# Kernel tuning notes

Measured on AMD Instinct MI355X. Metric: run time of the kernel, lower is better.

The kernel has to match this reference:

```python
import jax, jax.numpy as jnp
import numpy as np

B, S, D, H = 2, 2048, 1024, 16
DK = D // H
ROPE_BASE = 10000.0


def setup_inputs() -> dict:
    key = jax.random.key(0)
    ks = jax.random.split(key, 6)
    x = jax.random.normal(ks[0], (B, S, D), dtype=jnp.float32)
    # causal mask, broadcastable to [B,H,S,S]; masked_fill where mask==0
    mask = jnp.tril(jnp.ones((S, S), dtype=bool))[None, None]
    position_ids = jnp.tile(jnp.arange(S, dtype=jnp.int32)[None, :], (B, 1))
    sc = 1.0 / np.sqrt(D)
    Wq = jax.random.normal(ks[1], (D, D), dtype=jnp.float32) * sc
    Wk = jax.random.normal(ks[2], (D, D), dtype=jnp.float32) * sc
    Wv = jax.random.normal(ks[3], (D, D), dtype=jnp.float32) * sc
    Wo = jax.random.normal(ks[4], (D, D), dtype=jnp.float32) * sc
    bo = jnp.zeros((D,), dtype=jnp.float32)
    return {"x": x, "mask": mask, "position_ids": position_ids,
            "Wq": Wq, "Wk": Wk, "Wv": Wv, "Wo": Wo, "bo": bo}


def _rotate_half(t):
    t1, t2 = t[..., : t.shape[-1] // 2], t[..., t.shape[-1] // 2:]
    return jnp.concatenate((-t2, t1), axis=-1)


def reference(x, mask, position_ids, Wq, Wk, Wv, Wo, bo):
    b, s, d = x.shape
    h, dk = H, DK
    scale = 1.0 / np.sqrt(dk)

    def proj(W):  # torch Linear: x @ W.T -> [b,h,s,dk]
        return (x @ W.T).reshape(b, s, h, dk).transpose(0, 2, 1, 3)

    Q, K, V = proj(Wq), proj(Wk), proj(Wv)

    # rotary tables (computed in fp32, matching RotaryEmbedding)
    inv_freq = 1.0 / (ROPE_BASE ** (jnp.arange(0, dk, 2, dtype=jnp.float32) / dk))
    t = jnp.arange(s, dtype=jnp.float32)
    freqs = jnp.outer(t, inv_freq)            # [s, dk/2]
    emb = jnp.concatenate((freqs, freqs), -1) # [s, dk]
    cos = jnp.cos(emb)[position_ids][:, None]  # [b,1,s,dk]
    sin = jnp.sin(emb)[position_ids][:, None]
    Q = Q * cos + _rotate_half(Q) * sin
    K = K * cos + _rotate_half(K) * sin

    scores = jnp.einsum('bhqd,bhkd->bhqk', Q, K) * scale
    scores = jnp.where(mask, scores, jnp.float32(-1e9))
    attn = jax.nn.softmax(scores, axis=-1)  # dropout is identity in eval
    out = jnp.einsum('bhqk,bhkd->bhqd', attn, V)
    out = out.transpose(0, 2, 1, 3).reshape(b, s, d)
    return out @ Wo.T + bo
```

## Files before the change

### kernel.cpp

```cpp
#include <hip/hip_runtime.h>
#include <hip/hip_bf16.h>
#include <cstdint>

#define BB 2
#define SS 2048
#define DD 1024
#define HH 16
#define DK 64
#define MROWS (BB*SS)
#define NQKV  (3*DD)

typedef __bf16 bf16x8 __attribute__((ext_vector_type(8)));
typedef float  f32x4  __attribute__((ext_vector_type(4)));
typedef float  f32x16 __attribute__((ext_vector_type(16)));
typedef unsigned u32x2 __attribute__((ext_vector_type(2)));

static __device__ __forceinline__ unsigned short f2bf(float f) {
    __bf16 h = (__bf16)f;
    return __builtin_bit_cast(unsigned short, h);
}
static __device__ __forceinline__ float bf2f(unsigned short u) {
    return (float)__builtin_bit_cast(__bf16, u);
}

#define GLOAD16(gsrc, ldst) \
    __builtin_amdgcn_global_load_lds((const __attribute__((address_space(1))) void*)(gsrc), \
                                     (__attribute__((address_space(3))) void*)(ldst), 16, 0, 0)

static __device__ __forceinline__ void pl32_swap(unsigned &x, unsigned &y) {
#if __has_builtin(__builtin_amdgcn_permlane32_swap)
    u32x2 r = __builtin_amdgcn_permlane32_swap(x, y, false, false);
    x = r[0]; y = r[1];
#else
    asm volatile("v_permlane32_swap_b32 %0, %1" : "+v"(x), "+v"(y));
#endif
}
static __device__ __forceinline__ float swap_half(float v, bool hi) {
    unsigned x = __builtin_bit_cast(unsigned, v), y = x;
    pl32_swap(x, y);
    return __builtin_bit_cast(float, hi ? x : y);
}
template<int BASE> static __device__ __forceinline__ bf16x8 cvt_chunk(const f32x16 &p) {
    unsigned x0, y0, x1, y1;
    asm("v_cvt_pk_bf16_f32 %0, %1, %2" : "=v"(x0) : "v"(p[BASE+0]), "v"(p[BASE+1]));
    asm("v_cvt_pk_bf16_f32 %0, %1, %2" : "=v"(y0) : "v"(p[BASE+4]), "v"(p[BASE+5]));
    asm("v_cvt_pk_bf16_f32 %0, %1, %2" : "=v"(x1) : "v"(p[BASE+2]), "v"(p[BASE+3]));
    asm("v_cvt_pk_bf16_f32 %0, %1, %2" : "=v"(y1) : "v"(p[BASE+6]), "v"(p[BASE+7]));
    pl32_swap(x0, y0);
    pl32_swap(x1, y1);
    union { unsigned u[4]; bf16x8 v; } r;
    r.u[0] = x0; r.u[1] = x1; r.u[2] = y0; r.u[3] = y1;
    return r.v;
}

__global__ void cast_all(const float* __restrict__ x,  const float* __restrict__ wq,
                         const float* __restrict__ wk, const float* __restrict__ wv,
                         const float* __restrict__ wo,
                         unsigned short* __restrict__ xb, unsigned short* __restrict__ wqkv,
                         unsigned short* __restrict__ wob)
{
    const int NX = MROWS * DD;
    const int NW = DD * DD;
    const int total = (NX + 4 * NW) / 8;
    for (int i = blockIdx.x * blockDim.x + threadIdx.x; i < total; i += gridDim.x * blockDim.x) {
        int base = i * 8;
        const float* src; unsigned short* dst; int off;
        if      (base < NX)          { src = x;  dst = xb;          off = base; }
        else if (base < NX + NW)     { src = wq; dst = wqkv;        off = base - NX; }
        else if (base < NX + 2*NW)   { src = wk; dst = wqkv + NW;   off = base - NX - NW; }
        else if (base < NX + 3*NW)   { src = wv; dst = wqkv + 2*NW; off = base - NX - 2*NW; }
        else                         { src = wo; dst = wob;         off = base - NX - 3*NW; }
        float4 a = *(const float4*)(src + off);
        float4 b = *(const float4*)(src + off + 4);
        union { unsigned short s[8]; uint4 v; } u;
        u.s[0] = f2bf(a.x); u.s[1] = f2bf(a.y); u.s[2] = f2bf(a.z); u.s[3] = f2bf(a.w);
        u.s[4] = f2bf(b.x); u.s[5] = f2bf(b.y); u.s[6] = f2bf(b.z); u.s[7] = f2bf(b.w);
        *(uint4*)(dst + off) = u.v;
    }
}

__global__ void rope_table(float* __restrict__ tabc, float* __restrict__ tabs)
{
    int i = blockIdx.x * blockDim.x + threadIdx.x;
    int s = i >> 5, d = i & 31;
    float inv = exp2f(-(float)d * (13.287712379549449f / 32.f));
    float ang = (float)s * inv;
    tabc[i] = cosf(ang);
    tabs[i] = sinf(ang);
}

__global__ __launch_bounds__(512) void gemm_qkv(
    const unsigned short* __restrict__ A, const unsigned short* __restrict__ Bm,
    const int* __restrict__ pids,
    const float* __restrict__ tabc, const float* __restrict__ tabs,
    unsigned short* __restrict__ Qb, unsigned short* __restrict__ Kb,
    unsigned short* __restrict__ Vr)
{
    __shared__ __align__(16) unsigned short sA[2][16384];
    __shared__ __align__(16) unsigned short sB[2][16384];
    const int tid = threadIdx.x;
    const int w = tid >> 6, l = tid & 63;
    const int wm = w >> 2, wn = w & 3;
    const int lr = l & 15, lg = l >> 4;
    const int swz = (blockIdx.x & 7) * 24 + (blockIdx.x >> 3);
    const int bx = swz % 12, by = swz / 12;
    const int mBase = by * 256;
    const int sr  = tid >> 3;
    const int scb = (tid & 7) * 8;
    const int sksw = scb ^ ((sr & 7) * 8);
    const int rdsw = (lr & 7) * 8;

    f32x4 acc[8][4] = {};

    auto stage = [&](int kt, int bb) {
        #pragma unroll
        for (int r = 0; r < 4; ++r) {
            GLOAD16(A  + (size_t)(mBase + r*64 + sr) * DD + kt + sksw,
                    &sA[bb][r*4096 + sr*64 + scb]);
            GLOAD16(Bm + (size_t)(bx*256 + r*64 + sr) * DD + kt + sksw,
                    &sB[bb][r*4096 + sr*64 + scb]);
        }
    };

    stage(0, 0);
    __syncthreads();

    for (int t = 0; t < 16; ++t) {
        const int cur = t & 1;
        #pragma unroll
        for (int p = 0; p < 4; ++p) {
            const int rh = p & 1, ks = p >> 1;
            bf16x8 af[4], bfv[4];
            #pragma unroll
            for (int rf = 0; rf < 4; ++rf) {
                int ra = wm*128 + rh*64 + rf*16 + lr;
                af[rf] = *(const bf16x8*)&sA[cur][ra*64 + ((ks*32 + lg*8) ^ rdsw)];
            }
            #pragma unroll
            for (int cf = 0; cf < 4; ++cf) {
                int rb = wn*64 + cf*16 + lr;
                bfv[cf] = *(const bf16x8*)&sB[cur][rb*64 + ((ks*32 + lg*8) ^ rdsw)];
            }
            if (p == 0 && t < 15) stage((t+1)*64, cur ^ 1);
            __builtin_amdgcn_s_barrier();
            __builtin_amdgcn_s_setprio(1);
            #pragma unroll
            for (int rf = 0; rf < 4; ++rf)
                #pragma unroll
                for (int cf = 0; cf < 4; ++cf)
                    acc[rh*4+rf][cf] = __builtin_amdgcn_mfma_f32_16x16x32_bf16(
                        af[rf], bfv[cf], acc[rh*4+rf][cf], 0, 0, 0);
            __builtin_amdgcn_s_setprio(0);
            if (p < 3) __builtin_amdgcn_s_barrier();
        }
        __syncthreads();
    }

    if (bx < 8) {
        const bool isQ = bx < 4;
        unsigned short* dst = isQ ? Qb : Kb;
        const float qsc = isQ ? 0.1803368801111244f : 1.0f;
        const int colbase = (bx & 3)*256 + wn*64;
        #pragma unroll
        for (int rr = 0; rr < 8; ++rr) {
            #pragma unroll
            for (int j = 0; j < 4; ++j) {
                int row = mBase + wm*128 + rr*16 + lg*4 + j;
                int pos = pids[row];
                #pragma unroll
                for (int cf = 0; cf < 2; ++cf) {
                    int d = cf*16 + lr;
                    float cc = tabc[pos*32 + d];
                    float sn = tabs[pos*32 + d];
                    float a  = acc[rr][cf][j];
                    float bb2 = acc[rr][cf+2][j];
                    dst[(size_t)row * DD + colbase + d]      = f2bf((a*cc - bb2*sn) * qsc);
                    dst[(size_t)row * DD + colbase + d + 32] = f2bf((bb2*cc + a*sn) * qsc);
                }
            }
        }
    } else {
        const int colbase = (bx - 8)*256 + wn*64;
        #pragma unroll
        for (int rr = 0; rr < 8; ++rr) {
            #pragma unroll
            for (int j = 0; j < 4; ++j) {
                int row = mBase + wm*128 + rr*16 + lg*4 + j;
                #pragma unroll
                for (int cf = 0; cf < 4; ++cf)
                    Vr[(size_t)row * DD + colbase + cf*16 + lr] = f2bf(acc[rr][cf][j]);
            }
        }
    }
}

__global__ __launch_bounds__(256) void gemm_bt(
    const unsigned short* __restrict__ A, const unsigned short* __restrict__ Bm,
    float* __restrict__ Cout, const float* __restrict__ bias,
    int M, int N, int K)
{
    __shared__ __align__(16) unsigned short sA[2][128 * 64];
    __shared__ __align__(16) unsigned short sB[2][128 * 64];
    const int tid = threadIdx.x;
    const int w = tid >> 6, l = tid & 63;
    const int wm = w >> 1, wn = w & 1;
    const int lr = l & 15, lg = l >> 4;
    const int nwg = gridDim.x;
    const int cpx = nwg >> 3;
    const int swz = (blockIdx.x & 7) * cpx + (blockIdx.x >> 3);
    const int nbx = N >> 7;
    const int bx = swz % nbx, by = swz / nbx;
    const int mBase = by * 128, nBase = bx * 128;
    const int srow = tid >> 3;
    const int skof = (tid & 7) * 8;

    f32x4 acc[4][4] = {};

    #pragma unroll
    for (int i = 0; i < 4; ++i) {
        GLOAD16(A  + (size_t)(mBase + i*32 + srow) * K + skof, &sA[0][i*2048 + w*512]);
        GLOAD16(Bm + (size_t)(nBase + i*32 + srow) * K + skof, &sB[0][i*2048 + w*512]);
    }
    int cur = 0;

    for (int kt = 0; kt < K; kt += 64) {
        __syncthreads();
        if (kt + 64 < K) {
            #pragma unroll
            for (int i = 0; i < 4; ++i) {
                GLOAD16(A  + (size_t)(mBase + i*32 + srow) * K + kt + 64 + skof, &sA[cur^1][i*2048 + w*512]);
                GLOAD16(Bm + (size_t)(nBase + i*32 + srow) * K + kt + 64 + skof, &sB[cur^1][i*2048 + w*512]);
            }
        }
        #pragma unroll
        for (int kk = 0; kk < 2; ++kk) {
            bf16x8 af[4], bfv[4];
            #pragma unroll
            for (int mi = 0; mi < 4; ++mi)
                af[mi] = *(const bf16x8*)&sA[cur][(wm*64 + mi*16 + lr)*64 + kk*32 + lg*8];
            #pragma unroll
            for (int ni = 0; ni < 4; ++ni)
                bfv[ni] = *(const bf16x8*)&sB[cur][(wn*64 + ni*16 + lr)*64 + kk*32 + lg*8];
            #pragma unroll
            for (int mi = 0; mi < 4; ++mi)
                #pragma unroll
                for (int ni = 0; ni < 4; ++ni)
                    acc[mi][ni] = __builtin_amdgcn_mfma_f32_16x16x32_bf16(af[mi], bfv[ni], acc[mi][ni], 0, 0, 0);
        }
        cur ^= 1;
    }
    #pragma unroll
    for (int mi = 0; mi < 4; ++mi) {
        #pragma unroll
        for (int j = 0; j < 4; ++j) {
            int row = mBase + wm*64 + mi*16 + lg*4 + j;
            #pragma unroll
            for (int ni = 0; ni < 4; ++ni) {
                int col = nBase + wn*64 + ni*16 + lr;
                Cout[(size_t)row * N + col] = acc[mi][ni][j] + bias[col];
            }
        }
    }
}

__global__ __launch_bounds__(256) void v_transpose(
    const unsigned short* __restrict__ Vr, unsigned short* __restrict__ Vt)
{
    __shared__ __align__(16) unsigned short sT[64 * 64];
    const int bh = blockIdx.y;
    const int st = blockIdx.x;
    const int b = bh >> 4, h = bh & 15;
    const int tid = threadIdx.x;
    #pragma unroll
    for (int i = 0; i < 2; ++i) {
        int c = tid + i*256;
        int s = c >> 3, cb = c & 7;
        const unsigned short* src = Vr + (size_t)(b*SS + st*64 + s) * DD + h*64 + cb*8;
        uint4 v = *(const uint4*)src;
        *(uint4*)&sT[s*64 + ((cb ^ (s >> 3)) * 8)] = v;
    }
    __syncthreads();
    #pragma unroll
    for (int i = 0; i < 2; ++i) {
        int c = tid + i*256;
        int d = c >> 3, sb = c & 7;
        union { unsigned short u[8]; uint4 v; } o;
        #pragma unroll
        for (int e = 0; e < 8; ++e) {
            int s = sb*8 + e;
            o.u[e] = sT[s*64 + (((d >> 3) ^ (s >> 3)) * 8) + (d & 7)];
        }
        *(uint4*)(Vt + (size_t)(bh*64 + d) * SS + st*64 + sb*8) = o.v;
    }
}

__global__ __launch_bounds__(256, 2) void attn_fwd(
    const unsigned short* __restrict__ Qb,
    const unsigned short* __restrict__ Kb,
    const unsigned short* __restrict__ Vt,
    unsigned short* __restrict__ Ob)
{
    __shared__ __align__(16) unsigned short sK[2][8192];
    __shared__ __align__(16) unsigned short sV[2][8192];
    const int tid = threadIdx.x;
    const int w = tid >> 6, l = tid & 63;
    const int lq = l & 31;
    const int hi5 = l >> 5;
    const bool hb = hi5 != 0;

    const int xcd  = blockIdx.x & 7;
    const int c    = blockIdx.x >> 3;
    const int gsel = c & 3;
    const int t    = c >> 2;
    const int qt   = (t < 8) ? t : 23 - t;
    const int bh   = xcd * 4 + gsel;
    const int b = bh >> 4, h = bh & 15;

    const int srow = tid >> 3;
    const int skof = (tid & 7) * 8;
    const int sksw = skof ^ ((srow & 7) * 8);
    const int sw   = (lq & 7) * 8;
    const float THR = 12.0f;

    bf16x8 qf[4];
    {
        const unsigned short* qp = Qb + (size_t)(b*SS + qt*128 + w*32 + lq) * DD + h*64 + hi5*8;
        #pragma unroll
        for (int dkc = 0; dkc < 4; ++dkc)
            qf[dkc] = *(const bf16x8*)(qp + dkc*16);
    }
    const int q_lane = qt*128 + w*32 + lq;
    const int wbase  = qt*128 + w*32;

    f32x16 o0 = {}, o1 = {};
    float mrow = -3.0e38f, lsum = 0.f;
    int cur = 0;

    auto stage = [&](int ktt, int bb) {
        #pragma unroll
        for (int r = 0; r < 4; ++r)
            GLOAD16(Kb + (size_t)(b*SS + ktt*128 + r*32 + srow) * DD + h*64 + sksw,
                    &sK[bb][r*2048 + w*512]);
        #pragma unroll
        for (int s = 0; s < 2; ++s)
            #pragma unroll
            for (int r = 0; r < 2; ++r)
                GLOAD16(Vt + (size_t)(bh*64 + r*32 + srow) * SS + ktt*128 + s*64 + sksw,
                        &sV[bb][s*4096 + r*2048 + w*512]);
    };

    stage(0, 0);

    for (int ktt = 0; ktt <= qt; ++ktt) {
        __syncthreads();
        if (ktt < qt) stage(ktt + 1, cur ^ 1);

        f32x16 pa0 = {}, pa1 = {};
        f32x16 pb0 = {}, pb1 = {};
        __builtin_amdgcn_s_setprio(1);
        #pragma unroll
        for (int dkc = 0; dkc < 4; ++dkc) {
            bf16x8 k0 = *(const bf16x8*)&sK[cur][lq*64 + ((dkc*16 + hi5*8) ^ sw)];
            pa0 = __builtin_amdgcn_mfma_f32_32x32x16_bf16(k0, qf[dkc], pa0, 0, 0, 0);
        }
        #pragma unroll
        for (int dkc = 0; dkc < 4; ++dkc) {
            bf16x8 k1 = *(const bf16x8*)&sK[cur][2048 + lq*64 + ((dkc*16 + hi5*8) ^ sw)];
            pa1 = __builtin_amdgcn_mfma_f32_32x32x16_bf16(k1, qf[dkc], pa1, 0, 0, 0);
        }
        #pragma unroll
        for (int dkc = 0; dkc < 4; ++dkc) {
            bf16x8 k2 = *(const bf16x8*)&sK[cur][4096 + lq*64 + ((dkc*16 + hi5*8) ^ sw)];
            pb0 = __builtin_amdgcn_mfma_f32_32x32x16_bf16(k2, qf[dkc], pb0, 0, 0, 0);
        }
        #pragma unroll
        for (int dkc = 0; dkc < 4; ++dkc) {
            bf16x8 k3 = *(const bf16x8*)&sK[cur][4096 + 2048 + lq*64 + ((dkc*16 + hi5*8) ^ sw)];
            pb1 = __builtin_amdgcn_mfma_f32_32x32x16_bf16(k3, qf[dkc], pb1, 0, 0, 0);
        }
        __builtin_amdgcn_s_setprio(0);

        {
            const int kt = 2*ktt;
            if (kt*64 + 63 > wbase) {
                const int kb0 = kt*64 + 4*hi5;
                #pragma unroll
                for (int r = 0; r < 16; ++r) {
                    const int cr = (r & 3) + 8*(r >> 2);
                    if (kb0 + cr > q_lane)      pa0[r] = -1e30f;
                    if (kb0 + 32 + cr > q_lane) pa1[r] = -1e30f;
                }
            }
            float tt[16];
            #pragma unroll
            for (int r = 0; r < 16; ++r) tt[r] = fmaxf(pa0[r], pa1[r]);
            #pragma unroll
            for (int s2 = 8; s2 >= 1; s2 >>= 1)
                #pragma unroll
                for (int r = 0; r < 8; ++r)
                    if (r < s2) tt[r] = fmaxf(tt[r], tt[r + s2]);
            float tmx = fmaxf(tt[0], swap_half(tt[0], hb));
            float growth = tmx - mrow;
            if (!__all(growth <= THR)) {
                float mnew = fmaxf(mrow, tmx);
                float alpha = exp2f(mrow - mnew);
                lsum *= alpha;
                mrow = mnew;
                #pragma unroll
                for (int r = 0; r < 16; ++r) { o0[r] *= alpha; o1[r] *= alpha; }
            }
            #pragma unroll
            for (int r = 0; r < 16; ++r) {
                pa0[r] = exp2f(pa0[r] - mrow);
                pa1[r] = exp2f(pa1[r] - mrow);
            }
            float st[16];
            #pragma unroll
            for (int r = 0; r < 16; ++r) st[r] = pa0[r] + pa1[r];
            #pragma unroll
            for (int s2 = 8; s2 >= 1; s2 >>= 1)
                #pragma unroll
                for (int r = 0; r < 8; ++r)
                    if (r < s2) st[r] += st[r + s2];
            lsum += st[0];
        }

        __builtin_amdgcn_s_setprio(1);
        {
            bf16x8 pv, vf;
            pv = cvt_chunk<0>(pa0);
            vf = *(const bf16x8*)&sV[cur][lq*64 + ((0*16 + hi5*8) ^ sw)];
            o0 = __builtin_amdgcn_mfma_f32_32x32x16_bf16(vf, pv, o0, 0, 0, 0);
            vf = *(const bf16x8*)&sV[cur][2048 + lq*64 + ((0*16 + hi5*8) ^ sw)];
            o1 = __builtin_amdgcn_mfma_f32_32x32x16_bf16(vf, pv, o1, 0, 0, 0);
            pv = cvt_chunk<8>(pa0);
            vf = *(const bf16x8*)&sV[cur][lq*64 + ((1*16 + hi5*8) ^ sw)];
            o0 = __builtin_amdgcn_mfma_f32_32x32x16_bf16(vf, pv, o0, 0, 0, 0);
            vf = *(const bf16x8*)&sV[cur][2048 + lq*64 + ((1*16 + hi5*8) ^ sw)];
            o1 = __builtin_amdgcn_mfma_f32_32x32x16_bf16(vf, pv, o1, 0, 0, 0);
            pv = cvt_chunk<0>(pa1);
            vf = *(const bf16x8*)&sV[cur][lq*64 + ((2*16 + hi5*8) ^ sw)];
            o0 = __builtin_amdgcn_mfma_f32_32x32x16_bf16(vf, pv, o0, 0, 0, 0);
            vf = *(const bf16x8*)&sV[cur][2048 + lq*64 + ((2*16 + hi5*8) ^ sw)];
            o1 = __builtin_amdgcn_mfma_f32_32x32x16_bf16(vf, pv, o1, 0, 0, 0);
            pv = cvt_chunk<8>(pa1);
            vf = *(const bf16x8*)&sV[cur][lq*64 + ((3*16 + hi5*8) ^ sw)];
            o0 = __builtin_amdgcn_mfma_f32_32x32x16_bf16(vf, pv, o0, 0, 0, 0);
            vf = *(const bf16x8*)&sV[cur][2048 + lq*64 + ((3*16 + hi5*8) ^ sw)];
            o1 = __builtin_amdgcn_mfma_f32_32x32x16_bf16(vf, pv, o1, 0, 0, 0);
        }
        __builtin_amdgcn_s_setprio(0);

        {
            const int kt = 2*ktt + 1;
            if (kt*64 + 63 > wbase) {
                const int kb0 = kt*64 + 4*hi5;
                #pragma unroll
                for (int r = 0; r < 16; ++r) {
                    const int cr = (r & 3) + 8*(r >> 2);
                    if (kb0 + cr > q_lane)      pb0[r] = -1e30f;
                    if (kb0 + 32 + cr > q_lane) pb1[r] = -1e30f;
                }
            }
            float tt[16];
            #pragma unroll
            for (int r = 0; r < 16; ++r) tt[r] = fmaxf(pb0[r], pb1[r]);
            #pragma unroll
            for (int s2 = 8; s2 >= 1; s2 >>= 1)
                #pragma unroll
                for (int r = 0; r < 8; ++r)
                    if (r < s2) tt[r] = fmaxf(tt[r], tt[r + s2]);
            float tmx = fmaxf(tt[0], swap_half(tt[0], hb));
            float growth = tmx - mrow;
            if (!__all(growth <= THR)) {
                float mnew = fmaxf(mrow, tmx);
                float alpha = exp2f(mrow - mnew);
                lsum *= alpha;
                mrow = mnew;
                #pragma unroll
                for (int r = 0; r < 16; ++r) { o0[r] *= alpha; o1[r] *= alpha; }
            }
            #pragma unroll
            for (int r = 0; r < 16; ++r) {
                pb0[r] = exp2f(pb0[r] - mrow);
                pb1[r] = exp2f(pb1[r] - mrow);
            }
            float st[16];
            #pragma unroll
            for (int r = 0; r < 16; ++r) st[r] = pb0[r] + pb1[r];
            #pragma unroll
            for (int s2 = 8; s2 >= 1; s2 >>= 1)
                #pragma unroll
                for (int r = 0; r < 8; ++r)
                    if (r < s2) st[r] += st[r + s2];
            lsum += st[0];
        }

        __builtin_amdgcn_s_setprio(1);
        {
            bf16x8 pv, vf;
            pv = cvt_chunk<0>(pb0);
            vf = *(const bf16x8*)&sV[cur][4096 + lq*64 + ((0*16 + hi5*8) ^ sw)];
            o0 = __builtin_amdgcn_mfma_f32_32x32x16_bf16(vf, pv, o0, 0, 0, 0);
            vf = *(const bf16x8*)&sV[cur][4096 + 2048 + lq*64 + ((0*16 + hi5*8) ^ sw)];
            o1 = __builtin_amdgcn_mfma_f32_32x32x16_bf16(vf, pv, o1, 0, 0, 0);
            pv = cvt_chunk<8>(pb0);
            vf = *(const bf16x8*)&sV[cur][4096 + lq*64 + ((1*16 + hi5*8) ^ sw)];
            o0 = __builtin_amdgcn_mfma_f32_32x32x16_bf16(vf, pv, o0, 0, 0, 0);
            vf = *(const bf16x8*)&sV[cur][4096 + 2048 + lq*64 + ((1*16 + hi5*8) ^ sw)];
            o1 = __builtin_amdgcn_mfma_f32_32x32x16_bf16(vf, pv, o1, 0, 0, 0);
            pv = cvt_chunk<0>(pb1);
            vf = *(const bf16x8*)&sV[cur][4096 + lq*64 + ((2*16 + hi5*8) ^ sw)];
            o0 = __builtin_amdgcn_mfma_f32_32x32x16_bf16(vf, pv, o0, 0, 0, 0);
            vf = *(const bf16x8*)&sV[cur][4096 + 2048 + lq*64 + ((2*16 + hi5*8) ^ sw)];
            o1 = __builtin_amdgcn_mfma_f32_32x32x16_bf16(vf, pv, o1, 0, 0, 0);
            pv = cvt_chunk<8>(pb1);
            vf = *(const bf16x8*)&sV[cur][4096 + lq*64 + ((3*16 + hi5*8) ^ sw)];
            o0 = __builtin_amdgcn_mfma_f32_32x32x16_bf16(vf, pv, o0, 0, 0, 0);
            vf = *(const bf16x8*)&sV[cur][4096 + 2048 + lq*64 + ((3*16 + hi5*8) ^ sw)];
            o1 = __builtin_amdgcn_mfma_f32_32x32x16_bf16(vf, pv, o1, 0, 0, 0);
        }
        __builtin_amdgcn_s_setprio(0);
        cur ^= 1;
    }

    __syncthreads();
    float ls = lsum + swap_half(lsum, hb);
    float inv = 1.f / ls;
    unsigned short* sOw = &sK[0][0] + w * 2048;

    #pragma unroll
    for (int g2 = 0; g2 < 4; ++g2) {
        unsigned ua, ub; uint2 t2;
        float v0 = o0[g2*4+0]*inv, v1 = o0[g2*4+1]*inv, v2 = o0[g2*4+2]*inv, v3 = o0[g2*4+3]*inv;
        asm("v_cvt_pk_bf16_f32 %0, %1, %2" : "=v"(ua) : "v"(v0), "v"(v1));
        asm("v_cvt_pk_bf16_f32 %0, %1, %2" : "=v"(ub) : "v"(v2), "v"(v3));
        t2.x = ua; t2.y = ub;
        *(uint2*)&sOw[lq*64 + g2*8 + hi5*4] = t2;
        float w0 = o1[g2*4+0]*inv, w1 = o1[g2*4+1]*inv, w2 = o1[g2*4+2]*inv, w3 = o1[g2*4+3]*inv;
        asm("v_cvt_pk_bf16_f32 %0, %1, %2" : "=v"(ua) : "v"(w0), "v"(w1));
        asm("v_cvt_pk_bf16_f32 %0, %1, %2" : "=v"(ub) : "v"(w2), "v"(w3));
        t2.x = ua; t2.y = ub;
        *(uint2*)&sOw[lq*64 + 32 + g2*8 + hi5*4] = t2;
    }
    asm volatile("s_waitcnt lgkmcnt(0)" ::: "memory");
    __builtin_amdgcn_sched_barrier(0);

    const int row = l >> 1, cb2 = (l & 1) * 32;
    const unsigned short* sOr = sOw + row*64 + cb2;
    unsigned short* gp = Ob + (size_t)(b*SS + qt*128 + w*32 + row) * DD + h*64 + cb2;
    #pragma unroll
    for (int c2 = 0; c2 < 4; ++c2)
        *(uint4*)(gp + c2*8) = *(const uint4*)(sOr + c2*8);
}

extern "C" void kernel_launch(void* const* d_in, const int* in_sizes, int n_in,
                              void* d_out, int out_size, void* d_ws, size_t ws_size,
                              hipStream_t stream)
{
    const float* x  = (const float*)d_in[0];
    const int* pids = (const int*)d_in[2];
    const float* wq = (const float*)d_in[3];
    const float* wk = (const float*)d_in[4];
    const float* wv = (const float*)d_in[5];
    const float* wo = (const float*)d_in[6];
    const float* bo = (const float*)d_in[7];
    float* out = (float*)d_out;

    char* ws = (char*)d_ws;
    unsigned short* xb   = (unsigned short*)(ws);
    unsigned short* wqkv = (unsigned short*)(ws + (size_t)( 8u<<20));
    unsigned short* wob  = (unsigned short*)(ws + (size_t)(14u<<20));
    unsigned short* Vr   = (unsigned short*)(ws + (size_t)(16u<<20));
    unsigned short* Qb   = (unsigned short*)(ws + (size_t)(40u<<20));
    unsigned short* Kb   = (unsigned short*)(ws + (size_t)(48u<<20));
    unsigned short* Vt   = (unsigned short*)(ws + (size_t)(56u<<20));
    float* tabc          = (float*)(ws + (size_t)(64u<<20));
    float* tabs          = (float*)(ws + (size_t)(64u<<20) + (256u<<10));
    unsigned short* Ob   = xb;

    cast_all<<<dim3(4096), dim3(256), 0, stream>>>(x, wq, wk, wv, wo, xb, wqkv, wob);
    rope_table<<<dim3(256), dim3(256), 0, stream>>>(tabc, tabs);
    gemm_qkv<<<dim3(192), dim3(512), 0, stream>>>(
        xb, wqkv, pids, tabc, tabs, Qb, Kb, Vr);
    v_transpose<<<dim3(32, 32), dim3(256), 0, stream>>>(Vr, Vt);
    attn_fwd<<<dim3(512), dim3(256), 0, stream>>>(Qb, Kb, Vt, Ob);
    gemm_bt<<<dim3(256), dim3(256), 0, stream>>>(
        Ob, wob, out, bo, MROWS, DD, DD);
}
```

Baseline: 133.9 us.

## Deepen QKV GEMM pipeline to four-slot K=32 ring with vmcnt waits

Replaces the double-buffered K=64 staging in the QKV projection GEMM with a four-slot ring of K=32 tiles, keeping three loads in flight. It uses s_waitcnt vmcnt counting and one barrier per step instead of full __syncthreads, and changes the LDS swizzle to fit 32-wide rows. The aim is to hide global-load latency better and cut synchronisation overhead. In exchange there are twice as many iterations, and the code relies on the vmcnt count matching the number of outstanding loads.

```diff
diff --git a/kernel.cpp b/kernel.cpp
--- a/kernel.cpp
+++ b/kernel.cpp
@@ -96,8 +96,8 @@
     unsigned short* __restrict__ Qb, unsigned short* __restrict__ Kb,
     unsigned short* __restrict__ Vr)
 {
-    __shared__ __align__(16) unsigned short sA[2][16384];
-    __shared__ __align__(16) unsigned short sB[2][16384];
+    __shared__ __align__(16) unsigned short sA[4][8192];
+    __shared__ __align__(16) unsigned short sB[4][8192];
     const int tid = threadIdx.x;
     const int w = tid >> 6, l = tid & 63;
     const int wm = w >> 2, wn = w & 3;
@@ -105,55 +105,51 @@
     const int swz = (blockIdx.x & 7) * 24 + (blockIdx.x >> 3);
     const int bx = swz % 12, by = swz / 12;
     const int mBase = by * 256;
-    const int sr  = tid >> 3;
-    const int scb = (tid & 7) * 8;
-    const int sksw = scb ^ ((sr & 7) * 8);
-    const int rdsw = (lr & 7) * 8;
+    const int nBase = bx * 256;
+    const int srow = tid >> 2;
+    const int schw = tid & 3;
 
     f32x4 acc[8][4] = {};
 
-    auto stage = [&](int kt, int bb) {
-        #pragma unroll
-        for (int r = 0; r < 4; ++r) {
-            GLOAD16(A  + (size_t)(mBase + r*64 + sr) * DD + kt + sksw,
-                    &sA[bb][r*4096 + sr*64 + scb]);
-            GLOAD16(Bm + (size_t)(bx*256 + r*64 + sr) * DD + kt + sksw,
-                    &sB[bb][r*4096 + sr*64 + scb]);
+    auto stage = [&](int kh) {
+        const int slot = kh & 3;
+        const int kbase = kh * 32;
+        #pragma unroll
+        for (int r = 0; r < 2; ++r) {
+            int row = r * 128 + srow;
+            int scol = kbase + ((schw ^ ((row >> 1) & 3)) * 8);
+            GLOAD16(A  + (size_t)(mBase + row) * DD + scol, &sA[slot][r*4096 + tid*8]);
+            GLOAD16(Bm + (size_t)(nBase + row) * DD + scol, &sB[slot][r*4096 + tid*8]);
         }
     };
 
-    stage(0, 0);
-    __syncthreads();
-
-    for (int t = 0; t < 16; ++t) {
-        const int cur = t & 1;
-        #pragma unroll
-        for (int p = 0; p < 4; ++p) {
-            const int rh = p & 1, ks = p >> 1;
-            bf16x8 af[4], bfv[4];
-            #pragma unroll
-            for (int rf = 0; rf < 4; ++rf) {
-                int ra = wm*128 + rh*64 + rf*16 + lr;
-                af[rf] = *(const bf16x8*)&sA[cur][ra*64 + ((ks*32 + lg*8) ^ rdsw)];
-            }
-            #pragma unroll
-            for (int cf = 0; cf < 4; ++cf) {
-                int rb = wn*64 + cf*16 + lr;
-                bfv[cf] = *(const bf16x8*)&sB[cur][rb*64 + ((ks*32 + lg*8) ^ rdsw)];
-            }
-            if (p == 0 && t < 15) stage((t+1)*64, cur ^ 1);
-            __builtin_amdgcn_s_barrier();
-            __builtin_amdgcn_s_setprio(1);
-            #pragma unroll
-            for (int rf = 0; rf < 4; ++rf)
-                #pragma unroll
-                for (int cf = 0; cf < 4; ++cf)
-                    acc[rh*4+rf][cf] = __builtin_amdgcn_mfma_f32_16x16x32_bf16(
-                        af[rf], bfv[cf], acc[rh*4+rf][cf], 0, 0, 0);
-            __builtin_amdgcn_s_setprio(0);
-            if (p < 3) __builtin_amdgcn_s_barrier();
-        }
-        __syncthreads();
+    stage(0); stage(1); stage(2);
+
+    for (int n = 0; n < 32; ++n) {
+        if (n == 31) { asm volatile("s_waitcnt vmcnt(0)" ::: "memory"); }
+        else         { asm volatile("s_waitcnt vmcnt(8)" ::: "memory"); }
+        __builtin_amdgcn_s_barrier();
+        if (n + 3 < 32) stage(n + 3);
+        const int slot = n & 3;
+        bf16x8 af[8], bfv[4];
+        #pragma unroll
+        for (int rf = 0; rf < 8; ++rf) {
+            int ra = wm*128 + rf*16 + lr;
+            af[rf] = *(const bf16x8*)&sA[slot][ra*32 + ((lg ^ ((ra >> 1) & 3)) * 8)];
+        }
+        #pragma unroll
+        for (int cf = 0; cf < 4; ++cf) {
+            int rb = wn*64 + cf*16 + lr;
+            bfv[cf] = *(const bf16x8*)&sB[slot][rb*32 + ((lg ^ ((rb >> 1) & 3)) * 8)];
+        }
+        __builtin_amdgcn_s_setprio(1);
+        #pragma unroll
+        for (int rf = 0; rf < 8; ++rf)
+            #pragma unroll
+            for (int cf = 0; cf < 4; ++cf)
+                acc[rf][cf] = __builtin_amdgcn_mfma_f32_16x16x32_bf16(
+                    af[rf], bfv[cf], acc[rf][cf], 0, 0, 0);
+        __builtin_amdgcn_s_setprio(0);
     }
 
     if (bx < 8) {
```

Measured after the change: 137.6 us. 1.03x slower.

## Retile QKV GEMM to 256x192 tiles so 256 blocks fill all CUs

Applied to the files above, without the earlier changes.

The QKV projection GEMM moves from 256x256 output tiles (192 blocks, 8 waves) to 256x192 tiles (256 blocks, 6 waves in a 2x3 layout). The point is to match the 256 compute units on MI355X and remove the partial-wave tail left by 192 blocks. Staging becomes a flat loop with bounds checks over A and B chunks, and the epilogue works out the Q/K/V region from the global column. Each 64-column wave slice stays inside one head, so the RoPE pairing still holds, but reuse per block drops a little and the staging code gains branches.

```diff
diff --git a/kernel.cpp b/kernel.cpp
--- a/kernel.cpp
+++ b/kernel.cpp
@@ -89,7 +89,7 @@
     tabs[i] = sinf(ang);
 }
 
-__global__ __launch_bounds__(512) void gemm_qkv(
+__global__ __launch_bounds__(384) void gemm_qkv(
     const unsigned short* __restrict__ A, const unsigned short* __restrict__ Bm,
     const int* __restrict__ pids,
     const float* __restrict__ tabc, const float* __restrict__ tabs,
@@ -97,28 +97,33 @@
     unsigned short* __restrict__ Vr)
 {
     __shared__ __align__(16) unsigned short sA[2][16384];
-    __shared__ __align__(16) unsigned short sB[2][16384];
+    __shared__ __align__(16) unsigned short sB[2][12288];
     const int tid = threadIdx.x;
-    const int w = tid >> 6, l = tid & 63;
-    const int wm = w >> 2, wn = w & 3;
+    const int w = tid / 64, l = tid & 63;
+    const int wm = w / 3, wn = w % 3;
     const int lr = l & 15, lg = l >> 4;
-    const int swz = (blockIdx.x & 7) * 24 + (blockIdx.x >> 3);
-    const int bx = swz % 12, by = swz / 12;
+    const int swz = (blockIdx.x & 7) * 32 + (blockIdx.x >> 3);
+    const int bx = swz & 15, by = swz >> 4;
     const int mBase = by * 256;
-    const int sr  = tid >> 3;
-    const int scb = (tid & 7) * 8;
-    const int sksw = scb ^ ((sr & 7) * 8);
+    const int nBase = bx * 192;
     const int rdsw = (lr & 7) * 8;
 
     f32x4 acc[8][4] = {};
 
     auto stage = [&](int kt, int bb) {
         #pragma unroll
-        for (int r = 0; r < 4; ++r) {
-            GLOAD16(A  + (size_t)(mBase + r*64 + sr) * DD + kt + sksw,
-                    &sA[bb][r*4096 + sr*64 + scb]);
-            GLOAD16(Bm + (size_t)(bx*256 + r*64 + sr) * DD + kt + sksw,
-                    &sB[bb][r*4096 + sr*64 + scb]);
+        for (int r = 0; r < 10; ++r) {
+            int idx = tid + r * 384;
+            if (idx < 2048) {
+                int row = idx >> 3, ch = idx & 7;
+                GLOAD16(A + (size_t)(mBase + row) * DD + kt + ((ch ^ (row & 7)) * 8),
+                        &sA[bb][idx * 8]);
+            } else if (idx < 3584) {
+                int i2 = idx - 2048;
+                int row = i2 >> 3, ch = i2 & 7;
+                GLOAD16(Bm + (size_t)(nBase + row) * DD + kt + ((ch ^ (row & 7)) * 8),
+                        &sB[bb][i2 * 8]);
+            }
         }
     };
 
@@ -156,11 +161,12 @@
         __syncthreads();
     }
 
-    if (bx < 8) {
-        const bool isQ = bx < 4;
-        unsigned short* dst = isQ ? Qb : Kb;
-        const float qsc = isQ ? 0.1803368801111244f : 1.0f;
-        const int colbase = (bx & 3)*256 + wn*64;
+    const int gcol = nBase + wn*64;
+    const int region = gcol >> 10;
+    const int hcol = gcol & 1023;
+    if (region < 2) {
+        unsigned short* dst = (region == 0) ? Qb : Kb;
+        const float qsc = (region == 0) ? 0.1803368801111244f : 1.0f;
         #pragma unroll
         for (int rr = 0; rr < 8; ++rr) {
             #pragma unroll
@@ -174,13 +180,12 @@
                     float sn = tabs[pos*32 + d];
                     float a  = acc[rr][cf][j];
                     float bb2 = acc[rr][cf+2][j];
-                    dst[(size_t)row * DD + colbase + d]      = f2bf((a*cc - bb2*sn) * qsc);
-                    dst[(size_t)row * DD + colbase + d + 32] = f2bf((bb2*cc + a*sn) * qsc);
+                    dst[(size_t)row * DD + hcol + d]      = f2bf((a*cc - bb2*sn) * qsc);
+                    dst[(size_t)row * DD + hcol + d + 32] = f2bf((bb2*cc + a*sn) * qsc);
                 }
             }
         }
     } else {
-        const int colbase = (bx - 8)*256 + wn*64;
         #pragma unroll
         for (int rr = 0; rr < 8; ++rr) {
             #pragma unroll
@@ -188,7 +193,7 @@
                 int row = mBase + wm*128 + rr*16 + lg*4 + j;
                 #pragma unroll
                 for (int cf = 0; cf < 4; ++cf)
-                    Vr[(size_t)row * DD + colbase + cf*16 + lr] = f2bf(acc[rr][cf][j]);
+                    Vr[(size_t)row * DD + hcol + cf*16 + lr] = f2bf(acc[rr][cf][j]);
             }
         }
     }
@@ -581,7 +586,7 @@
 
     cast_all<<<dim3(4096), dim3(256), 0, stream>>>(x, wq, wk, wv, wo, xb, wqkv, wob);
     rope_table<<<dim3(256), dim3(256), 0, stream>>>(tabc, tabs);
-    gemm_qkv<<<dim3(192), dim3(512), 0, stream>>>(
+    gemm_qkv<<<dim3(256), dim3(384), 0, stream>>>(
         xb, wqkv, pids, tabc, tabs, Qb, Kb, Vr);
     v_transpose<<<dim3(32, 32), dim3(256), 0, stream>>>(Vr, Vt);
     attn_fwd<<<dim3(512), dim3(256), 0, stream>>>(Qb, Kb, Vt, Ob);
```

New measurement: 131.7 us. About the same (-1.7%).
